# Kernel tuning notes

Measured on AMD Instinct MI355X. Metric: run time of the kernel, lower is better.

Reference implementation:

```python
import jax, jax.numpy as jnp
import numpy as np
import math

NUM_BUCKETS = 32
MAX_DISTANCE = 128
NUM_HEADS = 16
D_MODEL = 1024
HEAD_DIM = D_MODEL // NUM_HEADS


def _relative_position_bucket(relative_position, num_buckets=NUM_BUCKETS, max_distance=MAX_DISTANCE):
    # bidirectional=False path of the original
    rp = -jnp.minimum(relative_position, 0)  # non-negative distances
    max_exact = num_buckets // 2
    is_small = rp < max_exact
    rp_safe = jnp.maximum(rp, 1).astype(jnp.float32)
    rp_if_large = max_exact + (
        jnp.log(rp_safe / max_exact) / math.log(max_distance / max_exact) * (num_buckets - max_exact)
    ).astype(jnp.int32)
    rp_if_large = jnp.minimum(rp_if_large, num_buckets - 1)
    return jnp.where(is_small, rp, rp_if_large)


def relative_bias(rab_weight, q_len, k_len):
    ctx = jnp.arange(q_len)[:, None]
    mem = jnp.arange(k_len)[None, :]
    buckets = _relative_position_bucket(mem - ctx)  # [Q, K]
    vals = rab_weight[buckets]                       # [Q, K, H]
    return jnp.transpose(vals, (2, 0, 1))[None]      # [1, H, Q, K]


def setup_inputs() -> dict:
    key = jax.random.key(0)
    k1, k2, k3, k4 = jax.random.split(key, 4)
    B, S = 4, 2048
    return {
        "v": jax.random.normal(k1, (B, S, D_MODEL), dtype=jnp.float32),
        "k": jax.random.normal(k2, (B, S, D_MODEL), dtype=jnp.float32),
        "q": jax.random.normal(k3, (B, S, D_MODEL), dtype=jnp.float32),
        "rab_weight": jax.random.normal(k4, (NUM_BUCKETS, NUM_HEADS), dtype=jnp.float32),
    }


def reference(v, k, q, rab_weight):
    B, S, _ = q.shape
    def split(x):
        return jnp.transpose(x.reshape(B, S, NUM_HEADS, HEAD_DIM), (0, 2, 1, 3))  # [B,H,S,D]
    qh, kh, vh = split(q), split(k), split(v)
    scores = jnp.einsum("bhqd,bhkd->bhqk", qh, kh)          # [B,H,S,S]
    scores = scores + relative_bias(rab_weight, S, S)        # add relative bias
    av = jnp.einsum("bhqk,bhkd->bhqd", jax.nn.silu(scores), vh)
    return jnp.transpose(av, (0, 2, 1, 3)).reshape(B, S, D_MODEL)
```

## Files before the change

kernel.cpp:

```cpp
#include <hip/hip_runtime.h>

#define NB 4
#define SEQ 2048
#define NH 16
#define HD 64
#define DMODEL 1024

typedef short bf16x8 __attribute__((ext_vector_type(8)));
typedef float f32x16 __attribute__((ext_vector_type(16)));

union FragU {
    bf16x8 v;
    uint2 u2[2];
    unsigned int w[4];
    unsigned short s[8];
};

#if __has_builtin(__builtin_amdgcn_cvt_pk_bf16_f32)
typedef __bf16 v2bf_t __attribute__((ext_vector_type(2)));
__device__ __forceinline__ unsigned int pack_bf16(float lo, float hi) {
    union { v2bf_t h; unsigned int u; } cv;
    cv.h = __builtin_amdgcn_cvt_pk_bf16_f32(lo, hi);
    return cv.u;
}
#else
__device__ __forceinline__ unsigned int pack_bf16(float lo, float hi) {
    unsigned int a = __float_as_uint(lo) + 0x8000u;
    unsigned int b = __float_as_uint(hi) + 0x8000u;
    return __builtin_amdgcn_perm(b, a, 0x07060302);
}
#endif

#define EXP_SCALE 1.44269504f
#define LN2       0.69314718f

__global__ __launch_bounds__(512, 4)
void paa_kernel(const float* __restrict__ Vg, const float* __restrict__ Kg,
                const float* __restrict__ Qg, const float* __restrict__ RW,
                float* __restrict__ Og)
{
    __shared__ __align__(16) unsigned short KsLds[64 * 68];
    __shared__ __align__(16) unsigned short VtLds[64 * 68];
    __shared__ float btab[128];

    const int tid  = threadIdx.x;
    const int lane = tid & 63;
    const int wave = tid >> 6;
    const int half = lane >> 5;
    const int l31  = lane & 31;

    const int bid  = blockIdx.x;
    const int bh   = bid & 63;
    const int qt   = bid >> 6;
    const int b    = bh >> 4;
    const int head = bh & 15;

    const int q0w = qt * 256 + wave * 32;

    if (tid < 128) {
        int rp = tid;
        int bucket;
        if (rp < 16) bucket = rp;
        else {
            int big = 16 + (int)(logf((float)rp * 0.0625f) * 7.6943736f);
            bucket = big < 31 ? big : 31;
        }
        btab[tid] = RW[bucket * NH + head] * EXP_SCALE;
    }

    FragU qf[4];
    {
        const float* qrow = Qg + (size_t)(b * SEQ + q0w + l31) * DMODEL + head * HD;
        #pragma unroll
        for (int kf = 0; kf < 4; ++kf) {
            int dd = kf * 16 + half * 8;
            float4 x0 = *(const float4*)(qrow + dd);
            float4 x1 = *(const float4*)(qrow + dd + 4);
            FragU f;
            f.w[0] = pack_bf16(x0.x * EXP_SCALE, x0.y * EXP_SCALE);
            f.w[1] = pack_bf16(x0.z * EXP_SCALE, x0.w * EXP_SCALE);
            f.w[2] = pack_bf16(x1.x * EXP_SCALE, x1.y * EXP_SCALE);
            f.w[3] = pack_bf16(x1.z * EXP_SCALE, x1.w * EXP_SCALE);
            qf[kf] = f;
        }
    }

    f32x16 oacc[2];
    #pragma unroll
    for (int n = 0; n < 2; ++n)
        #pragma unroll
        for (int r = 0; r < 16; ++r) oacc[n][r] = 0.0f;

    __syncthreads();
    const float bias_d0  = btab[0];
    const float bias_far = btab[127];

    const int krow = tid >> 4;
    const int c4   = tid & 15;
    const int kc2  = tid >> 4;
    const int d4   = tid & 15;

    const float* kbase = Kg + (size_t)(b * SEQ) * DMODEL + head * HD;
    const float* vbase = Vg + (size_t)(b * SEQ) * DMODEL + head * HD;

    for (int it = 0; it < 32; ++it) {
        const int kcb = it * 64;

        #pragma unroll
        for (int i = 0; i < 2; ++i) {
            int row = krow + i * 32;
            float4 x = *(const float4*)(kbase + (size_t)(kcb + row) * DMODEL + c4 * 4);
            uint2 w;
            w.x = pack_bf16(x.x, x.y);
            w.y = pack_bf16(x.z, x.w);
            *(uint2*)&KsLds[row * 68 + c4 * 4] = w;
        }
        {
            const float* vrow = vbase + (size_t)(kcb + kc2 * 2) * DMODEL + d4 * 4;
            float4 x0 = *(const float4*)(vrow);
            float4 x1 = *(const float4*)(vrow + DMODEL);
            *(unsigned int*)&VtLds[(d4 * 4 + 0) * 68 + kc2 * 2] = pack_bf16(x0.x, x1.x);
            *(unsigned int*)&VtLds[(d4 * 4 + 1) * 68 + kc2 * 2] = pack_bf16(x0.y, x1.y);
            *(unsigned int*)&VtLds[(d4 * 4 + 2) * 68 + kc2 * 2] = pack_bf16(x0.z, x1.z);
            *(unsigned int*)&VtLds[(d4 * 4 + 3) * 68 + kc2 * 2] = pack_bf16(x0.w, x1.w);
        }
        __syncthreads();

        FragU pf[4];
        #pragma unroll
        for (int t = 0; t < 2; ++t) {
            const int kcmin = kcb + t * 32;
            FragU ka[4];
            #pragma unroll
            for (int kf = 0; kf < 4; ++kf) {
                int off = (t * 32 + l31) * 68 + kf * 16 + half * 8;
                ka[kf].u2[0] = *(const uint2*)&KsLds[off];
                ka[kf].u2[1] = *(const uint2*)&KsLds[off + 4];
            }
            f32x16 st;
            if (q0w + 31 - kcmin <= 0) {
                #pragma unroll
                for (int r = 0; r < 16; ++r) st[r] = bias_d0;
            } else if (q0w - (kcmin + 31) >= 113) {
                #pragma unroll
                for (int r = 0; r < 16; ++r) st[r] = bias_far;
            } else {
                const int dql = q0w + l31 - kcmin - 4 * half;
                #pragma unroll
                for (int r = 0; r < 16; ++r) {
                    int dv = dql - ((r & 3) + 8 * (r >> 2));
                    dv = dv < 0 ? 0 : (dv > 127 ? 127 : dv);
                    st[r] = btab[dv];
                }
            }
            #pragma unroll
            for (int kf = 0; kf < 4; ++kf)
                st = __builtin_amdgcn_mfma_f32_32x32x16_bf16(ka[kf].v, qf[kf].v, st, 0, 0, 0);

            float vals[16];
            #pragma unroll
            for (int r = 0; r < 16; ++r) {
                float x = st[r];
                float e = __builtin_amdgcn_exp2f(-x);
                vals[r] = x * __builtin_amdgcn_rcpf(1.0f + e);
            }
            #pragma unroll
            for (int j = 0; j < 4; ++j)
                pf[t * 2].w[j]     = pack_bf16(vals[2 * j], vals[2 * j + 1]);
            #pragma unroll
            for (int j = 0; j < 4; ++j)
                pf[t * 2 + 1].w[j] = pack_bf16(vals[8 + 2 * j], vals[9 + 2 * j]);
        }

        #pragma unroll
        for (int f = 0; f < 4; ++f) {
            #pragma unroll
            for (int n = 0; n < 2; ++n) {
                FragU vf;
                int off = (n * 32 + l31) * 68 + f * 16 + half * 4;
                vf.u2[0] = *(const uint2*)&VtLds[off];
                vf.u2[1] = *(const uint2*)&VtLds[off + 8];
                oacc[n] = __builtin_amdgcn_mfma_f32_32x32x16_bf16(pf[f].v, vf.v, oacc[n], 0, 0, 0);
            }
        }
        __syncthreads();
    }

    float* obase = Og + (size_t)(b * SEQ) * DMODEL + head * HD;
    #pragma unroll
    for (int r = 0; r < 16; ++r) {
        int q = q0w + (r & 3) + 8 * (r >> 2) + 4 * half;
        float* orow = obase + (size_t)q * DMODEL;
        #pragma unroll
        for (int n = 0; n < 2; ++n)
            orow[n * 32 + l31] = oacc[n][r] * LN2;
    }
}

extern "C" void kernel_launch(void* const* d_in, const int* in_sizes, int n_in,
                              void* d_out, int out_size, void* d_ws, size_t ws_size,
                              hipStream_t stream) {
    const float* v  = (const float*)d_in[0];
    const float* k  = (const float*)d_in[1];
    const float* q  = (const float*)d_in[2];
    const float* rw = (const float*)d_in[3];
    float* out = (float*)d_out;
    paa_kernel<<<dim3(512), dim3(512), 0, stream>>>(v, k, q, rw, out);
}
```

Measured before the change: 229.8 us.

## Double-buffer K/V tiles in LDS with register prefetch and one barrier

Adds a second LDS buffer for the K and V tiles. The next tile's global loads are issued into registers at the start of each iteration and written to the other buffer after the softmax stage. This hides global load latency behind the MFMA work and drops one of the two barriers per iteration. It also interleaves the two score MFMA chains, wraps them in s_setprio, and unrolls the loop by two, at the cost of more registers and twice the LDS per block, which may lower occupancy.

```diff
diff --git a/kernel.cpp b/kernel.cpp
--- a/kernel.cpp
+++ b/kernel.cpp
@@ -1,6 +1,5 @@
 #include <hip/hip_runtime.h>
 
-#define NB 4
 #define SEQ 2048
 #define NH 16
 #define HD 64
@@ -39,8 +38,8 @@
                 const float* __restrict__ Qg, const float* __restrict__ RW,
                 float* __restrict__ Og)
 {
-    __shared__ __align__(16) unsigned short KsLds[64 * 68];
-    __shared__ __align__(16) unsigned short VtLds[64 * 68];
+    __shared__ __align__(16) unsigned short KsLds[2][64 * 68];
+    __shared__ __align__(16) unsigned short VtLds[2][64 * 68];
     __shared__ float btab[128];
 
     const int tid  = threadIdx.x;
@@ -91,76 +90,99 @@
         #pragma unroll
         for (int r = 0; r < 16; ++r) oacc[n][r] = 0.0f;
 
-    __syncthreads();
-    const float bias_d0  = btab[0];
-    const float bias_far = btab[127];
-
     const int krow = tid >> 4;
     const int c4   = tid & 15;
     const int kc2  = tid >> 4;
     const int d4   = tid & 15;
 
-    const float* kbase = Kg + (size_t)(b * SEQ) * DMODEL + head * HD;
-    const float* vbase = Vg + (size_t)(b * SEQ) * DMODEL + head * HD;
-
+    const float* kp = Kg + (size_t)(b * SEQ + krow) * DMODEL + head * HD + c4 * 4;
+    const float* vp = Vg + (size_t)(b * SEQ + kc2 * 2) * DMODEL + head * HD + d4 * 4;
+
+    {
+        float4 k0 = *(const float4*)(kp);
+        float4 k1 = *(const float4*)(kp + (size_t)32 * DMODEL);
+        float4 v0 = *(const float4*)(vp);
+        float4 v1 = *(const float4*)(vp + DMODEL);
+        kp += (size_t)64 * DMODEL;
+        vp += (size_t)64 * DMODEL;
+        uint2 w;
+        w.x = pack_bf16(k0.x, k0.y); w.y = pack_bf16(k0.z, k0.w);
+        *(uint2*)&KsLds[0][krow * 68 + c4 * 4] = w;
+        w.x = pack_bf16(k1.x, k1.y); w.y = pack_bf16(k1.z, k1.w);
+        *(uint2*)&KsLds[0][(krow + 32) * 68 + c4 * 4] = w;
+        *(unsigned int*)&VtLds[0][(d4 * 4 + 0) * 68 + kc2 * 2] = pack_bf16(v0.x, v1.x);
+        *(unsigned int*)&VtLds[0][(d4 * 4 + 1) * 68 + kc2 * 2] = pack_bf16(v0.y, v1.y);
+        *(unsigned int*)&VtLds[0][(d4 * 4 + 2) * 68 + kc2 * 2] = pack_bf16(v0.z, v1.z);
+        *(unsigned int*)&VtLds[0][(d4 * 4 + 3) * 68 + kc2 * 2] = pack_bf16(v0.w, v1.w);
+    }
+    __syncthreads();
+
+    const float bias_d0  = btab[0];
+    const float bias_far = btab[127];
+
+    #pragma unroll 2
     for (int it = 0; it < 32; ++it) {
+        const int cur = it & 1;
         const int kcb = it * 64;
-
-        #pragma unroll
-        for (int i = 0; i < 2; ++i) {
-            int row = krow + i * 32;
-            float4 x = *(const float4*)(kbase + (size_t)(kcb + row) * DMODEL + c4 * 4);
-            uint2 w;
-            w.x = pack_bf16(x.x, x.y);
-            w.y = pack_bf16(x.z, x.w);
-            *(uint2*)&KsLds[row * 68 + c4 * 4] = w;
-        }
-        {
-            const float* vrow = vbase + (size_t)(kcb + kc2 * 2) * DMODEL + d4 * 4;
-            float4 x0 = *(const float4*)(vrow);
-            float4 x1 = *(const float4*)(vrow + DMODEL);
-            *(unsigned int*)&VtLds[(d4 * 4 + 0) * 68 + kc2 * 2] = pack_bf16(x0.x, x1.x);
-            *(unsigned int*)&VtLds[(d4 * 4 + 1) * 68 + kc2 * 2] = pack_bf16(x0.y, x1.y);
-            *(unsigned int*)&VtLds[(d4 * 4 + 2) * 68 + kc2 * 2] = pack_bf16(x0.z, x1.z);
-            *(unsigned int*)&VtLds[(d4 * 4 + 3) * 68 + kc2 * 2] = pack_bf16(x0.w, x1.w);
-        }
-        __syncthreads();
-
-        FragU pf[4];
+        const unsigned short* Ks = KsLds[cur];
+        const unsigned short* Vt = VtLds[cur];
+        const bool pre = (it < 31);
+
+        float4 k0, k1, v0, v1;
+        if (pre) {
+            k0 = *(const float4*)(kp);
+            k1 = *(const float4*)(kp + (size_t)32 * DMODEL);
+            v0 = *(const float4*)(vp);
+            v1 = *(const float4*)(vp + DMODEL);
+            kp += (size_t)64 * DMODEL;
+            vp += (size_t)64 * DMODEL;
+        }
+
+        f32x16 st[2];
         #pragma unroll
         for (int t = 0; t < 2; ++t) {
             const int kcmin = kcb + t * 32;
-            FragU ka[4];
-            #pragma unroll
-            for (int kf = 0; kf < 4; ++kf) {
-                int off = (t * 32 + l31) * 68 + kf * 16 + half * 8;
-                ka[kf].u2[0] = *(const uint2*)&KsLds[off];
-                ka[kf].u2[1] = *(const uint2*)&KsLds[off + 4];
-            }
-            f32x16 st;
             if (q0w + 31 - kcmin <= 0) {
                 #pragma unroll
-                for (int r = 0; r < 16; ++r) st[r] = bias_d0;
+                for (int r = 0; r < 16; ++r) st[t][r] = bias_d0;
             } else if (q0w - (kcmin + 31) >= 113) {
                 #pragma unroll
-                for (int r = 0; r < 16; ++r) st[r] = bias_far;
+                for (int r = 0; r < 16; ++r) st[t][r] = bias_far;
             } else {
                 const int dql = q0w + l31 - kcmin - 4 * half;
                 #pragma unroll
                 for (int r = 0; r < 16; ++r) {
                     int dv = dql - ((r & 3) + 8 * (r >> 2));
                     dv = dv < 0 ? 0 : (dv > 127 ? 127 : dv);
-                    st[r] = btab[dv];
+                    st[t][r] = btab[dv];
                 }
             }
-            #pragma unroll
-            for (int kf = 0; kf < 4; ++kf)
-                st = __builtin_amdgcn_mfma_f32_32x32x16_bf16(ka[kf].v, qf[kf].v, st, 0, 0, 0);
-
+        }
+
+        __builtin_amdgcn_s_setprio(1);
+        #pragma unroll
+        for (int kf = 0; kf < 4; ++kf) {
+            FragU ka0, ka1;
+            {
+                int off = l31 * 68 + kf * 16 + half * 8;
+                ka0.u2[0] = *(const uint2*)&Ks[off];
+                ka0.u2[1] = *(const uint2*)&Ks[off + 4];
+                off += 32 * 68;
+                ka1.u2[0] = *(const uint2*)&Ks[off];
+                ka1.u2[1] = *(const uint2*)&Ks[off + 4];
+            }
+            st[0] = __builtin_amdgcn_mfma_f32_32x32x16_bf16(ka0.v, qf[kf].v, st[0], 0, 0, 0);
+            st[1] = __builtin_amdgcn_mfma_f32_32x32x16_bf16(ka1.v, qf[kf].v, st[1], 0, 0, 0);
+        }
+        __builtin_amdgcn_s_setprio(0);
+
+        FragU pf[4];
+        #pragma unroll
+        for (int t = 0; t < 2; ++t) {
             float vals[16];
             #pragma unroll
             for (int r = 0; r < 16; ++r) {
-                float x = st[r];
+                float x = st[t][r];
                 float e = __builtin_amdgcn_exp2f(-x);
                 vals[r] = x * __builtin_amdgcn_rcpf(1.0f + e);
             }
@@ -170,6 +192,19 @@
             #pragma unroll
             for (int j = 0; j < 4; ++j)
                 pf[t * 2 + 1].w[j] = pack_bf16(vals[8 + 2 * j], vals[9 + 2 * j]);
+        }
+
+        if (pre) {
+            const int nb = cur ^ 1;
+            uint2 w;
+            w.x = pack_bf16(k0.x, k0.y); w.y = pack_bf16(k0.z, k0.w);
+            *(uint2*)&KsLds[nb][krow * 68 + c4 * 4] = w;
+            w.x = pack_bf16(k1.x, k1.y); w.y = pack_bf16(k1.z, k1.w);
+            *(uint2*)&KsLds[nb][(krow + 32) * 68 + c4 * 4] = w;
+            *(unsigned int*)&VtLds[nb][(d4 * 4 + 0) * 68 + kc2 * 2] = pack_bf16(v0.x, v1.x);
+            *(unsigned int*)&VtLds[nb][(d4 * 4 + 1) * 68 + kc2 * 2] = pack_bf16(v0.y, v1.y);
+            *(unsigned int*)&VtLds[nb][(d4 * 4 + 2) * 68 + kc2 * 2] = pack_bf16(v0.z, v1.z);
+            *(unsigned int*)&VtLds[nb][(d4 * 4 + 3) * 68 + kc2 * 2] = pack_bf16(v0.w, v1.w);
         }
 
         #pragma unroll
@@ -178,12 +213,13 @@
             for (int n = 0; n < 2; ++n) {
                 FragU vf;
                 int off = (n * 32 + l31) * 68 + f * 16 + half * 4;
-                vf.u2[0] = *(const uint2*)&VtLds[off];
-                vf.u2[1] = *(const uint2*)&VtLds[off + 8];
+                vf.u2[0] = *(const uint2*)&Vt[off];
+                vf.u2[1] = *(const uint2*)&Vt[off + 8];
                 oacc[n] = __builtin_amdgcn_mfma_f32_32x32x16_bf16(pf[f].v, vf.v, oacc[n], 0, 0, 0);
             }
         }
-        __syncthreads();
+
+        if (pre) __syncthreads();
     }
 
     float* obase = Og + (size_t)(b * SEQ) * DMODEL + head * HD;
```

Result: faster. 214.7 us (-6.5%).
